# Kernel optimization log

Hardware: AMD Instinct MI355X
Metric: run time of the kernel (lower is better)

Reference implementation:

```python
import jax, jax.numpy as jnp
import numpy as np


def setup_inputs() -> dict:
    key = jax.random.key(0)
    ks = jax.random.split(key, 12)
    N, E, D_IN, D_H, R, B, G, C, D_E = 50000, 600000, 128, 128, 8, 4, 64, 16, 16
    x = jax.random.normal(ks[0], (N, D_IN), dtype=jnp.float32)
    edge_index = jax.random.randint(ks[1], (2, E), 0, N, dtype=jnp.int64)
    edge_type = jax.random.randint(ks[2], (E,), 0, R, dtype=jnp.int64)
    edge_attr = jax.random.normal(ks[3], (E, D_E), dtype=jnp.float32)
    batch = jnp.sort(jax.random.randint(ks[4], (N,), 0, G, dtype=jnp.int64))
    # RGCNConv basis-decomposition params + root + bias
    basis = jax.random.normal(ks[5], (B, D_IN, D_H), dtype=jnp.float32) / np.sqrt(D_IN)
    comp = jax.random.normal(ks[6], (R, B), dtype=jnp.float32) / np.sqrt(B)
    root = jax.random.normal(ks[7], (D_IN, D_H), dtype=jnp.float32) / np.sqrt(D_IN)
    bias = jnp.zeros((D_H,), dtype=jnp.float32)
    fc_w = jax.random.normal(ks[8], (D_H, C), dtype=jnp.float32) / np.sqrt(D_H)
    fc_b = jnp.zeros((C,), dtype=jnp.float32)
    return {"x": x, "edge_index": edge_index, "edge_type": edge_type,
            "edge_attr": edge_attr, "batch": batch, "num_graphs": 64,
            "basis": basis, "comp": comp, "root": root, "bias": bias,
            "fc_w": fc_w, "fc_b": fc_b}


def reference(x, edge_index, edge_type, edge_attr, batch, num_graphs,
              basis, comp, root, bias, fc_w, fc_b):
    N = x.shape[0]
    R = comp.shape[0]
    src, dst = edge_index[0], edge_index[1]
    # relation weights from basis decomposition: [R, in, out]
    W = jnp.einsum('rb,bio->rio', comp, basis)
    x_src = x[src]  # gather source features [E, in]
    agg = jnp.zeros((N, W.shape[2]), dtype=x.dtype)
    # per-relation mean aggregation (PyG RGCNConv default), summed over relations
    for r in range(R):
        mask = (edge_type == r).astype(x.dtype)  # [E]
        msg = (x_src @ W[r]) * mask[:, None]     # [E, out]
        summed = jax.ops.segment_sum(msg, dst, num_segments=N)
        cnt = jax.ops.segment_sum(mask, dst, num_segments=N)
        agg = agg + summed / jnp.maximum(cnt, 1.0)[:, None]
    h = jax.nn.relu(x @ root + bias + agg)       # [N, hidden]
    # global mean pool over graphs
    pooled_sum = jax.ops.segment_sum(h, batch, num_segments=num_graphs)
    gcnt = jax.ops.segment_sum(jnp.ones((N,), dtype=x.dtype), batch, num_segments=num_graphs)
    pooled = pooled_sum / jnp.maximum(gcnt, 1.0)[:, None]  # [G, hidden]
    return pooled @ fc_w + fc_b                  # [G, num_classes]
```

## Files before the change

### kernel.cpp

```cpp
#include <hip/hip_runtime.h>

static inline int ceil_div(int a, int b){ return (a+b-1)/b; }
static inline size_t align_up(size_t x, size_t a){ return (x + a - 1) / a * a; }

typedef __bf16 bf16x8 __attribute__((ext_vector_type(8)));
typedef float  f32x4  __attribute__((ext_vector_type(4)));

static __device__ inline unsigned short f2bf(float f){
    unsigned int u = __float_as_uint(f);
    unsigned int lsb = (u >> 16) & 1u;
    u += 0x7FFFu + lsb;
    return (unsigned short)(u >> 16);
}
static __device__ inline float bf2f(unsigned short b){
    return __uint_as_float(((unsigned int)b) << 16);
}
static __device__ inline unsigned int packbf(float a, float b){
    return (unsigned int)f2bf(a) | ((unsigned int)f2bf(b) << 16);
}

static __device__ inline void gload_lds16(const void* g, void* l) {
    __builtin_amdgcn_global_load_lds(
        (const __attribute__((address_space(1))) unsigned int*)g,
        (__attribute__((address_space(3))) unsigned int*)l, 16, 0, 0);
}

__global__ void compute_Bt_kernel(const float* __restrict__ comp, const float* __restrict__ basis,
                                  const float* __restrict__ root, unsigned short* __restrict__ Bt,
                                  int B) {
    int idx = blockIdx.x*blockDim.x + threadIdx.x;
    if (idx >= 128*1152) return;
    int o = idx / 1152, kk = idx - o*1152;
    float val;
    if (kk < 1024) {
        int r = kk >> 7, i = kk & 127;
        val = 0.f;
        for (int b = 0; b < B; ++b)
            val += comp[r*B+b] * basis[((size_t)b*128 + i)*128 + o];
    } else {
        val = root[(size_t)(kk-1024)*128 + o];
    }
    Bt[idx] = f2bf(val);
}

__global__ void count_kernel(const int* __restrict__ dst, const int* __restrict__ et,
                             int* __restrict__ cnt, int E, int R) {
    int e = blockIdx.x*blockDim.x + threadIdx.x;
    if (e >= E) return;
    atomicAdd(&cnt[(size_t)dst[e]*R + et[e]], 1);
}

__global__ __launch_bounds__(256)
void scan_block_kernel(const int* __restrict__ in, int* __restrict__ out,
                       int* __restrict__ bsums, int n) {
    __shared__ int tsum[256];
    int t = threadIdx.x;
    int idx0 = blockIdx.x*1024 + t*4;
    int v0 = (idx0+0 < n) ? in[idx0+0] : 0;
    int v1 = (idx0+1 < n) ? in[idx0+1] : 0;
    int v2 = (idx0+2 < n) ? in[idx0+2] : 0;
    int v3 = (idx0+3 < n) ? in[idx0+3] : 0;
    int s = v0+v1+v2+v3;
    tsum[t] = s; __syncthreads();
    for (int off = 1; off < 256; off <<= 1) {
        int x = (t >= off) ? tsum[t-off] : 0;
        __syncthreads();
        tsum[t] += x;
        __syncthreads();
    }
    int run = tsum[t] - s;
    if (idx0+0 < n) out[idx0+0] = run; run += v0;
    if (idx0+1 < n) out[idx0+1] = run; run += v1;
    if (idx0+2 < n) out[idx0+2] = run; run += v2;
    if (idx0+3 < n) out[idx0+3] = run;
    if (bsums && t == 255) bsums[blockIdx.x] = tsum[255];
}

__global__ void scan_add_kernel(int* __restrict__ out, const int* __restrict__ bs,
                                int n, int total) {
    int i = blockIdx.x*blockDim.x + threadIdx.x;
    if (i < n) out[i] += bs[i >> 10];
    if (i == 0) out[n] = total;
}

__global__ void fill_kernel(const int* __restrict__ src, const int* __restrict__ dst,
                            const int* __restrict__ et, int* __restrict__ offsets,
                            int* __restrict__ slot_src, int E, int R) {
    int e = blockIdx.x*blockDim.x + threadIdx.x;
    if (e >= E) return;
    int bin = dst[e]*R + et[e];
    int slot = atomicAdd(&offsets[bin], 1);
    slot_src[slot] = src[e];
}

__global__ __launch_bounds__(256)
void xb_kernel(const float* __restrict__ x, unsigned int* __restrict__ Xb2, int N) {
    int t = blockIdx.x*blockDim.x + threadIdx.x;
    int n = t >> 6;
    if (n >= N) return;
    int l = t & 63;
    float2 v = reinterpret_cast<const float2*>(x + (size_t)n*128)[l];
    Xb2[(size_t)n*64 + l] = packbf(v.x, v.y);
}

__global__ __launch_bounds__(256)
void aggregate_kernel(const int* __restrict__ offsets, const int* __restrict__ slot_src,
                      const unsigned int* __restrict__ Xb2, unsigned int* __restrict__ Mc2,
                      int N) {
    int gw = (int)((blockIdx.x*blockDim.x + threadIdx.x) >> 6);
    int node = gw >> 2, part = gw & 3;
    if (node >= N) return;
    int l = threadIdx.x & 63;
    int base = node*8 + part*2;
    int lo   = (base == 0) ? 0 : offsets[base-1];
    int bmid = offsets[base];
    int hi   = offsets[base+1];

    float ax0=0.f, ay0=0.f, ax1=0.f, ay1=0.f;

#define ACC2(E_, U_) { \
    float vx_ = bf2f((unsigned short)((U_) & 0xFFFFu)); \
    float vy_ = bf2f((unsigned short)((U_) >> 16)); \
    if ((E_) < bmid) { ax0 += vx_; ay0 += vy_; } \
    else             { ax1 += vx_; ay1 += vy_; } }

    int e = lo;
    for (; e + 4 <= hi; e += 4) {
        int s0 = slot_src[e], s1 = slot_src[e+1], s2 = slot_src[e+2], s3 = slot_src[e+3];
        unsigned int u0 = Xb2[(size_t)s0*64 + l];
        unsigned int u1 = Xb2[(size_t)s1*64 + l];
        unsigned int u2 = Xb2[(size_t)s2*64 + l];
        unsigned int u3 = Xb2[(size_t)s3*64 + l];
        ACC2(e+0, u0) ACC2(e+1, u1) ACC2(e+2, u2) ACC2(e+3, u3)
    }
    for (; e < hi; ++e) {
        int s = slot_src[e];
        unsigned int u = Xb2[(size_t)s*64 + l];
        ACC2(e, u)
    }
#undef ACC2

    unsigned int* Mrow = Mc2 + (size_t)node*512;
    float i0 = 1.f/fmaxf((float)(bmid-lo), 1.f);
    float i1 = 1.f/fmaxf((float)(hi-bmid), 1.f);
    Mrow[(2*part+0)*64 + l] = packbf(ax0*i0, ay0*i0);
    Mrow[(2*part+1)*64 + l] = packbf(ax1*i1, ay1*i1);
}

__global__ __launch_bounds__(256)
void mfma_gemm_kernel(const unsigned short* __restrict__ Mc,
                      const unsigned short* __restrict__ Xb,
                      const unsigned short* __restrict__ Btc,
                      const float* __restrict__ bias,
                      unsigned short* __restrict__ h) {
    __shared__ char ldsA[64*128];
    __shared__ char ldsB[128*128];

    int tid  = threadIdx.x;
    int lane = tid & 63;
    int wid  = tid >> 6;
    int rg = wid & 1, cg = wid >> 1;
    int fr = lane & 15, kb = lane >> 4;
    long m0 = (long)blockIdx.x * 64;

    int lrow8 = lane >> 3;
    int lcb   = (lane & 7) * 16;

    f32x4 acc[2][4];
    #pragma unroll
    for (int mf = 0; mf < 2; ++mf)
        #pragma unroll
        for (int nf = 0; nf < 4; ++nf) acc[mf][nf] = f32x4{0.f,0.f,0.f,0.f};

    const char* McB = (const char*)Mc;
    const char* XbB = (const char*)Xb;
    const char* BtB = (const char*)Btc;

    for (int t = 0; t < 18; ++t) {
        #pragma unroll
        for (int i = 0; i < 2; ++i) {
            int row = wid*16 + i*8 + lrow8;
            int sw  = lcb ^ ((row & 7) << 4);
            const char* g = (t < 16)
                ? McB + (size_t)(m0 + row)*2048 + t*128 + sw
                : XbB + (size_t)(m0 + row)*256 + (t-16)*128 + sw;
            gload_lds16(g, &ldsA[wid*2048 + i*1024 + lane*16]);
        }
        #pragma unroll
        for (int i = 0; i < 4; ++i) {
            int col = wid*32 + i*8 + lrow8;
            int sw  = lcb ^ ((col & 7) << 4);
            const char* g = BtB + (size_t)col*2304 + t*128 + sw;
            gload_lds16(g, &ldsB[wid*4096 + i*1024 + lane*16]);
        }
        __syncthreads();

        bf16x8 af[2][2], bf[4][2];
        #pragma unroll
        for (int mf = 0; mf < 2; ++mf) {
            int row = rg*32 + mf*16 + fr;
            #pragma unroll
            for (int kk = 0; kk < 2; ++kk) {
                int byte = row*128 + ((kk*64 + kb*16) ^ ((row & 7) << 4));
                af[mf][kk] = *reinterpret_cast<const bf16x8*>(&ldsA[byte]);
            }
        }
        #pragma unroll
        for (int nf = 0; nf < 4; ++nf) {
            int col = cg*64 + nf*16 + fr;
            #pragma unroll
            for (int kk = 0; kk < 2; ++kk) {
                int byte = col*128 + ((kk*64 + kb*16) ^ ((col & 7) << 4));
                bf[nf][kk] = *reinterpret_cast<const bf16x8*>(&ldsB[byte]);
            }
        }
        #pragma unroll
        for (int kk = 0; kk < 2; ++kk)
            #pragma unroll
            for (int mf = 0; mf < 2; ++mf)
                #pragma unroll
                for (int nf = 0; nf < 4; ++nf)
                    acc[mf][nf] = __builtin_amdgcn_mfma_f32_16x16x32_bf16(
                        af[mf][kk], bf[nf][kk], acc[mf][nf], 0, 0, 0);
        __syncthreads();
    }

    float bb[4];
    #pragma unroll
    for (int nf = 0; nf < 4; ++nf) bb[nf] = bias[cg*64 + nf*16 + fr];

    #pragma unroll
    for (int mf = 0; mf < 2; ++mf)
        #pragma unroll
        for (int q = 0; q < 4; ++q) {
            long r = m0 + rg*32 + mf*16 + kb*4 + q;
            unsigned short* hr = h + (size_t)r*128 + cg*64;
            #pragma unroll
            for (int nf = 0; nf < 4; ++nf)
                hr[nf*16 + fr] = f2bf(fmaxf(acc[mf][nf][q] + bb[nf], 0.f));
        }
}

__global__ __launch_bounds__(512)
void pool_fc_kernel(const unsigned int* __restrict__ h2, const int* __restrict__ batch,
                    const float* __restrict__ fw, const float* __restrict__ fb,
                    float* __restrict__ out, int N, int C) {
    int g = blockIdx.x;
    int t = threadIdx.x;
    int lo = 0, hi = N;
    while (lo < hi) { int mid = (lo+hi) >> 1; if (batch[mid] < g) lo = mid+1; else hi = mid; }
    int s0 = lo;
    hi = N;
    while (lo < hi) { int mid = (lo+hi) >> 1; if (batch[mid] < g+1) lo = mid+1; else hi = mid; }
    int s1 = lo;

    int d2 = t & 63;
    float ax = 0.f, ay = 0.f;
    for (int row = s0 + (t >> 6); row < s1; row += 8) {
        unsigned int u = h2[(size_t)row*64 + d2];
        ax += bf2f((unsigned short)(u & 0xFFFFu));
        ay += bf2f((unsigned short)(u >> 16));
    }
    __shared__ float ps[128];
    if (t < 128) ps[t] = 0.f;
    __syncthreads();
    atomicAdd(&ps[2*d2],   ax);
    atomicAdd(&ps[2*d2+1], ay);
    __syncthreads();
    if (t < C) {
        float inv = 1.f / fmaxf((float)(s1 - s0), 1.f);
        float s = 0.f;
        #pragma unroll 4
        for (int k = 0; k < 128; ++k) s += ps[k] * fw[(size_t)k*C + t];
        out[(size_t)g*C + t] = s * inv + fb[t];
    }
}

extern "C" void kernel_launch(void* const* d_in, const int* in_sizes, int n_in,
                              void* d_out, int out_size, void* d_ws, size_t ws_size,
                              hipStream_t stream) {
    const float* x       = (const float*)d_in[0];
    const int*   eindex  = (const int*)  d_in[1];
    const int*   etype   = (const int*)  d_in[2];
    const int*   batch   = (const int*)  d_in[4];
    const float* basis   = (const float*)d_in[6];
    const float* comp    = (const float*)d_in[7];
    const float* root    = (const float*)d_in[8];
    const float* bias    = (const float*)d_in[9];
    const float* fc_w    = (const float*)d_in[10];
    const float* fc_b    = (const float*)d_in[11];

    int N  = in_sizes[4];
    int E  = in_sizes[2];
    int C  = in_sizes[11];
    int G  = out_size / C;
    int IO = in_sizes[8];
    int B  = in_sizes[6] / IO;
    int R  = in_sizes[7] / B;
    int NR = N * R;
    int MB = ceil_div(N, 64);
    int Mpad = MB * 64;

    const int* src = eindex;
    const int* dst = eindex + E;

    char* base = (char*)d_ws;
    size_t off = 0;
    auto alloc = [&](size_t bytes) -> char* {
        char* p = base + off;
        off = align_up(off + bytes, 256);
        return p;
    };
    unsigned short* Bt  = (unsigned short*)alloc(sizeof(unsigned short)*128*1152);
    int*   cnt      = (int*)  alloc(sizeof(int)*(size_t)NR);
    int*   offsets  = (int*)  alloc(sizeof(int)*((size_t)NR+1));
    int*   bsums    = (int*)  alloc(sizeof(int)*1024);
    int*   slot_src = (int*)  alloc(sizeof(int)*(size_t)E);
    unsigned short* h  = (unsigned short*)alloc(sizeof(unsigned short)*(size_t)Mpad*128);
    unsigned short* Xb = (unsigned short*)alloc(sizeof(unsigned short)*(size_t)Mpad*128);
    unsigned short* Mc = (unsigned short*)alloc(sizeof(unsigned short)*(size_t)Mpad*1024);

    hipMemsetAsync(cnt, 0, sizeof(int)*(size_t)NR, stream);
    compute_Bt_kernel<<<ceil_div(128*1152,256),256,0,stream>>>(comp, basis, root, Bt, B);
    count_kernel<<<ceil_div(E,256),256,0,stream>>>(dst, etype, cnt, E, R);

    int nb = ceil_div(NR, 1024);
    scan_block_kernel<<<nb,256,0,stream>>>(cnt, offsets, bsums, NR);
    scan_block_kernel<<<1,256,0,stream>>>(bsums, bsums, nullptr, nb);
    scan_add_kernel<<<ceil_div(NR,256),256,0,stream>>>(offsets, bsums, NR, E);

    fill_kernel<<<ceil_div(E,256),256,0,stream>>>(src, dst, etype, offsets, slot_src, E, R);

    xb_kernel<<<ceil_div(N*64,256),256,0,stream>>>(x, (unsigned int*)Xb, N);
    aggregate_kernel<<<ceil_div(N*4*64,256),256,0,stream>>>(offsets, slot_src,
                                                            (const unsigned int*)Xb,
                                                            (unsigned int*)Mc, N);

    mfma_gemm_kernel<<<MB,256,0,stream>>>(Mc, Xb, Bt, bias, h);

    pool_fc_kernel<<<G,512,0,stream>>>((const unsigned int*)h, batch, fc_w, fc_b,
                                       (float*)d_out, N, C);
}
```

Baseline: 215.1 us.

## Fuse per-relation mean aggregation into the MFMA GEMM A-tile producer

The separate aggregation kernel, which wrote a bf16 N×1024 message buffer, is removed. The GEMM kernel now gathers and averages neighbour features per relation directly into its LDS A tile for each K-step, using CSR offsets cached in shared memory. This avoids writing and re-reading the large intermediate buffer, which is roughly 100 MB of traffic. In exchange the gather latency now sits inside the GEMM loop with no overlap against the MFMA work, and parallelism is limited to the GEMM's 782 blocks.

```diff
diff --git a/kernel.cpp b/kernel.cpp
--- a/kernel.cpp
+++ b/kernel.cpp
@@ -104,57 +104,14 @@
 }
 
 __global__ __launch_bounds__(256)
-void aggregate_kernel(const int* __restrict__ offsets, const int* __restrict__ slot_src,
-                      const unsigned int* __restrict__ Xb2, unsigned int* __restrict__ Mc2,
-                      int N) {
-    int gw = (int)((blockIdx.x*blockDim.x + threadIdx.x) >> 6);
-    int node = gw >> 2, part = gw & 3;
-    if (node >= N) return;
-    int l = threadIdx.x & 63;
-    int base = node*8 + part*2;
-    int lo   = (base == 0) ? 0 : offsets[base-1];
-    int bmid = offsets[base];
-    int hi   = offsets[base+1];
-
-    float ax0=0.f, ay0=0.f, ax1=0.f, ay1=0.f;
-
-#define ACC2(E_, U_) { \
-    float vx_ = bf2f((unsigned short)((U_) & 0xFFFFu)); \
-    float vy_ = bf2f((unsigned short)((U_) >> 16)); \
-    if ((E_) < bmid) { ax0 += vx_; ay0 += vy_; } \
-    else             { ax1 += vx_; ay1 += vy_; } }
-
-    int e = lo;
-    for (; e + 4 <= hi; e += 4) {
-        int s0 = slot_src[e], s1 = slot_src[e+1], s2 = slot_src[e+2], s3 = slot_src[e+3];
-        unsigned int u0 = Xb2[(size_t)s0*64 + l];
-        unsigned int u1 = Xb2[(size_t)s1*64 + l];
-        unsigned int u2 = Xb2[(size_t)s2*64 + l];
-        unsigned int u3 = Xb2[(size_t)s3*64 + l];
-        ACC2(e+0, u0) ACC2(e+1, u1) ACC2(e+2, u2) ACC2(e+3, u3)
-    }
-    for (; e < hi; ++e) {
-        int s = slot_src[e];
-        unsigned int u = Xb2[(size_t)s*64 + l];
-        ACC2(e, u)
-    }
-#undef ACC2
-
-    unsigned int* Mrow = Mc2 + (size_t)node*512;
-    float i0 = 1.f/fmaxf((float)(bmid-lo), 1.f);
-    float i1 = 1.f/fmaxf((float)(hi-bmid), 1.f);
-    Mrow[(2*part+0)*64 + l] = packbf(ax0*i0, ay0*i0);
-    Mrow[(2*part+1)*64 + l] = packbf(ax1*i1, ay1*i1);
-}
-
-__global__ __launch_bounds__(256)
-void mfma_gemm_kernel(const unsigned short* __restrict__ Mc,
-                      const unsigned short* __restrict__ Xb,
-                      const unsigned short* __restrict__ Btc,
-                      const float* __restrict__ bias,
-                      unsigned short* __restrict__ h) {
+void fused_gemm_kernel(const int* __restrict__ offsets, const int* __restrict__ slot_src,
+                       const unsigned short* __restrict__ Xb,
+                       const unsigned short* __restrict__ Btc,
+                       const float* __restrict__ bias,
+                       unsigned short* __restrict__ h, int NR_total) {
     __shared__ char ldsA[64*128];
     __shared__ char ldsB[128*128];
+    __shared__ int  lds_off[513];
 
     int tid  = threadIdx.x;
     int lane = tid & 63;
@@ -165,6 +122,20 @@
 
     int lrow8 = lane >> 3;
     int lcb   = (lane & 7) * 16;
+    int np = lane >> 5;
+    int fl = lane & 31;
+
+    const unsigned int* Xb2 = (const unsigned int*)Xb;
+
+    for (int k = tid; k < 513; k += 256) {
+        long gidx = m0*8 - 1 + k;
+        int v = 0;
+        if (gidx >= 0) {
+            long ci = gidx < (long)NR_total ? gidx : (long)NR_total;
+            v = offsets[ci];
+        }
+        lds_off[k] = v;
+    }
 
     f32x4 acc[2][4];
     #pragma unroll
@@ -172,20 +143,12 @@
         #pragma unroll
         for (int nf = 0; nf < 4; ++nf) acc[mf][nf] = f32x4{0.f,0.f,0.f,0.f};
 
-    const char* McB = (const char*)Mc;
     const char* XbB = (const char*)Xb;
     const char* BtB = (const char*)Btc;
 
+    __syncthreads();
+
     for (int t = 0; t < 18; ++t) {
-        #pragma unroll
-        for (int i = 0; i < 2; ++i) {
-            int row = wid*16 + i*8 + lrow8;
-            int sw  = lcb ^ ((row & 7) << 4);
-            const char* g = (t < 16)
-                ? McB + (size_t)(m0 + row)*2048 + t*128 + sw
-                : XbB + (size_t)(m0 + row)*256 + (t-16)*128 + sw;
-            gload_lds16(g, &ldsA[wid*2048 + i*1024 + lane*16]);
-        }
         #pragma unroll
         for (int i = 0; i < 4; ++i) {
             int col = wid*32 + i*8 + lrow8;
@@ -193,9 +156,64 @@
             const char* g = BtB + (size_t)col*2304 + t*128 + sw;
             gload_lds16(g, &ldsB[wid*4096 + i*1024 + lane*16]);
         }
+        if (t < 16) {
+            int r = t >> 1, fh = t & 1;
+            #pragma unroll
+            for (int pg = 0; pg < 2; ++pg) {
+                int lo[4], hi[4], sl[4][4];
+                #pragma unroll
+                for (int p4 = 0; p4 < 4; ++p4) {
+                    int nl = wid*16 + (pg*4 + p4)*2 + np;
+                    int bx = nl*8 + r;
+                    lo[p4] = lds_off[bx];
+                    hi[p4] = lds_off[bx+1];
+                    #pragma unroll
+                    for (int j = 0; j < 4; ++j) {
+                        int idx = lo[p4] + j;
+                        idx = idx < hi[p4]-1 ? idx : hi[p4]-1;
+                        idx = idx > 0 ? idx : 0;
+                        sl[p4][j] = slot_src[idx];
+                    }
+                }
+                unsigned int uv[4][4];
+                #pragma unroll
+                for (int p4 = 0; p4 < 4; ++p4)
+                    #pragma unroll
+                    for (int j = 0; j < 4; ++j)
+                        uv[p4][j] = Xb2[(size_t)sl[p4][j]*64 + fh*32 + fl];
+                #pragma unroll
+                for (int p4 = 0; p4 < 4; ++p4) {
+                    int nl = wid*16 + (pg*4 + p4)*2 + np;
+                    float ax = 0.f, ay = 0.f;
+                    #pragma unroll
+                    for (int j = 0; j < 4; ++j) {
+                        unsigned int u = (lo[p4] + j < hi[p4]) ? uv[p4][j] : 0u;
+                        ax += bf2f((unsigned short)(u & 0xFFFFu));
+                        ay += bf2f((unsigned short)(u >> 16));
+                    }
+                    for (int e = lo[p4] + 4; e < hi[p4]; ++e) {
+                        int s = slot_src[e];
+                        unsigned int u = Xb2[(size_t)s*64 + fh*32 + fl];
+                        ax += bf2f((unsigned short)(u & 0xFFFFu));
+                        ay += bf2f((unsigned short)(u >> 16));
+                    }
+                    float inv = 1.f / fmaxf((float)(hi[p4]-lo[p4]), 1.f);
+                    int byte = nl*128 + ((fl*4) ^ ((nl & 7) << 4));
+                    *(unsigned int*)&ldsA[byte] = packbf(ax*inv, ay*inv);
+                }
+            }
+        } else {
+            #pragma unroll
+            for (int i = 0; i < 2; ++i) {
+                int row = wid*16 + i*8 + lrow8;
+                int sw  = lcb ^ ((row & 7) << 4);
+                const char* g = XbB + (size_t)(m0 + row)*256 + (t-16)*128 + sw;
+                gload_lds16(g, &ldsA[wid*2048 + i*1024 + lane*16]);
+            }
+        }
         __syncthreads();
 
-        bf16x8 af[2][2], bf[4][2];
+        bf16x8 af[2][2], bfr[4][2];
         #pragma unroll
         for (int mf = 0; mf < 2; ++mf) {
             int row = rg*32 + mf*16 + fr;
@@ -211,7 +229,7 @@
             #pragma unroll
             for (int kk = 0; kk < 2; ++kk) {
                 int byte = col*128 + ((kk*64 + kb*16) ^ ((col & 7) << 4));
-                bf[nf][kk] = *reinterpret_cast<const bf16x8*>(&ldsB[byte]);
+                bfr[nf][kk] = *reinterpret_cast<const bf16x8*>(&ldsB[byte]);
             }
         }
         #pragma unroll
@@ -221,7 +239,7 @@
                 #pragma unroll
                 for (int nf = 0; nf < 4; ++nf)
                     acc[mf][nf] = __builtin_amdgcn_mfma_f32_16x16x32_bf16(
-                        af[mf][kk], bf[nf][kk], acc[mf][nf], 0, 0, 0);
+                        af[mf][kk], bfr[nf][kk], acc[mf][nf], 0, 0, 0);
         __syncthreads();
     }
 
@@ -318,7 +336,6 @@
     int*   slot_src = (int*)  alloc(sizeof(int)*(size_t)E);
     unsigned short* h  = (unsigned short*)alloc(sizeof(unsigned short)*(size_t)Mpad*128);
     unsigned short* Xb = (unsigned short*)alloc(sizeof(unsigned short)*(size_t)Mpad*128);
-    unsigned short* Mc = (unsigned short*)alloc(sizeof(unsigned short)*(size_t)Mpad*1024);
 
     hipMemsetAsync(cnt, 0, sizeof(int)*(size_t)NR, stream);
     compute_Bt_kernel<<<ceil_div(128*1152,256),256,0,stream>>>(comp, basis, root, Bt, B);
@@ -332,11 +349,8 @@
     fill_kernel<<<ceil_div(E,256),256,0,stream>>>(src, dst, etype, offsets, slot_src, E, R);
 
     xb_kernel<<<ceil_div(N*64,256),256,0,stream>>>(x, (unsigned int*)Xb, N);
-    aggregate_kernel<<<ceil_div(N*4*64,256),256,0,stream>>>(offsets, slot_src,
-                                                            (const unsigned int*)Xb,
-                                                            (unsigned int*)Mc, N);
-
-    mfma_gemm_kernel<<<MB,256,0,stream>>>(Mc, Xb, Bt, bias, h);
+
+    fused_gemm_kernel<<<MB,256,0,stream>>>(offsets, slot_src, Xb, Bt, bias, h, NR);
 
     pool_fc_kernel<<<G,512,0,stream>>>((const unsigned int*)h, batch, fc_w, fc_b,
                                        (float*)d_out, N, C);
```

New measurement: 262.8 us. +22.1%, slower.
